# Kernel optimization log

Hardware: AMD Instinct MI355X
Metric: run time of the kernel (lower is better)

The kernel has to match this reference:

```python
import jax, jax.numpy as jnp
import numpy as np
import math

WS = 8           # window size
NUM_HEADS = 8
LN_EPS = 1e-5


def window_partition(x, ws):
    # x: [B, H, W, C] -> [B*nH*nW, ws, ws, C]
    B, H, W, C = x.shape
    x = x.reshape(B, H // ws, ws, W // ws, ws, C)
    return x.transpose(0, 1, 3, 2, 4, 5).reshape(-1, ws, ws, C)


def window_reverse(w, ws, H, W):
    # w: [B*nH*nW, ws, ws, C] -> [B, H, W, C]
    B = w.shape[0] // ((H // ws) * (W // ws))
    x = w.reshape(B, H // ws, W // ws, ws, ws, -1)
    return x.transpose(0, 1, 3, 2, 4, 5).reshape(B, H, W, -1)


def layernorm(x, g, b):
    mu = jnp.mean(x, axis=-1, keepdims=True)
    var = jnp.mean(jnp.square(x - mu), axis=-1, keepdims=True)
    return (x - mu) * jax.lax.rsqrt(var + LN_EPS) * g + b


def rotation_grid(H, W, ws):
    """Vectorized rotation_process lookup table -> sampling grid [H, W, 2]=(lat,lon)."""
    nH, nW = H // ws, W // ws
    r = 1.0 / ws
    seq = -1.0 + r + 2.0 * r * jnp.arange(ws, dtype=jnp.float32)  # make_coord centers
    ch, cw = jnp.meshgrid(seq, seq, indexing='ij')
    t0 = ch.reshape(-1) / nH                       # [ws*ws] latitude template
    t1 = cw.reshape(-1) / nW                       # [ws*ws] longitude template
    beta = (2.0 * (jnp.arange(nH, dtype=jnp.float32) + 0.5) / nH - 1.0) * (math.pi / 2)  # [nH]
    th = t0 * (math.pi / 2) + math.pi / 2
    ph = t1 * math.pi
    sb, cb = jnp.sin(beta)[:, None], jnp.cos(beta)[:, None]
    st, ct = jnp.sin(th)[None, :], jnp.cos(th)[None, :]
    sp, cp = jnp.sin(ph)[None, :], jnp.cos(ph)[None, :]
    new_th = jnp.arccos(-sb * st * cp + cb * ct)                    # [nH, ws*ws]
    new_ph = jnp.arctan2(st * sp, cb * st * cp + sb * ct)
    lat = jnp.clip((new_th - math.pi / 2) / (math.pi / 2), -1.0, 1.0)
    lon = new_ph / math.pi
    shift = 2.0 * (0.5 - (jnp.arange(nW, dtype=jnp.float32) + 0.5) / nW)
    lon = lon[:, None, :] - shift[None, :, None]                    # [nH, nW, ws*ws]
    lon = jnp.where(lon > 1.0, lon - 2.0, lon)
    lon = jnp.where(lon < -1.0, lon + 2.0, lon)
    lat = jnp.broadcast_to(lat[:, None, :], lon.shape)
    g = jnp.stack([lat, lon], axis=-1).reshape(nH, nW, ws, ws, 2)
    return g.transpose(0, 2, 1, 3, 4).reshape(H, W, 2)


def grid_sample_nearest(im, grid):
    """F.grid_sample(mode='nearest', align_corners=False, padding='zeros').
    im: [B, H, W, C]; grid: [H, W, 2]=(y,x) normalized; shared across batch."""
    B, H, W, C = im.shape
    gy, gx = grid[..., 0], grid[..., 1]
    iy = jnp.round(((gy + 1.0) * H - 1.0) / 2.0).astype(jnp.int32)
    ix = jnp.round(((gx + 1.0) * W - 1.0) / 2.0).astype(jnp.int32)
    valid = (iy >= 0) & (iy < H) & (ix >= 0) & (ix < W)
    iyc = jnp.clip(iy, 0, H - 1)
    ixc = jnp.clip(ix, 0, W - 1)
    out = im[:, iyc, ixc, :]                                        # [B, H, W, C]
    return out * valid[None, :, :, None].astype(im.dtype)


def dwconv3x3(x, w, b):
    # x: [B, C, H, W], w: [C, 1, 3, 3] depthwise
    y = jax.lax.conv_general_dilated(x, w, (1, 1), 'SAME',
                                     feature_group_count=x.shape[1],
                                     dimension_numbers=('NCHW', 'OIHW', 'NCHW'))
    return y + b[None, :, None, None]


def setup_inputs() -> dict:
    key = jax.random.key(0)
    B, H, W, C, dff = 8, 64, 128, 256, 1024
    ks = jax.random.split(key, 10)
    s = 0.02
    return {
        'x': jax.random.normal(ks[0], (B, H * W, C), jnp.float32),
        'H': H, 'W': W,
        'norm1_g': jnp.ones((C,), jnp.float32),
        'norm1_b': jnp.zeros((C,), jnp.float32),
        'wq': jax.random.normal(ks[1], (C, C), jnp.float32) * s,
        'bq': jnp.zeros((C,), jnp.float32),
        'wk': jax.random.normal(ks[2], (C, C), jnp.float32) * s,
        'bk': jnp.zeros((C,), jnp.float32),
        'wv': jax.random.normal(ks[3], (C, C), jnp.float32) * s,
        'bv': jnp.zeros((C,), jnp.float32),
        'rpe_w': jax.random.normal(ks[4], (C, 1, 3, 3), jnp.float32) * s,
        'rpe_b': jnp.zeros((C,), jnp.float32),
        'proj_w': jax.random.normal(ks[5], (C, C), jnp.float32) * s,
        'proj_b': jnp.zeros((C,), jnp.float32),
        'norm2_g': jnp.ones((C,), jnp.float32),
        'norm2_b': jnp.zeros((C,), jnp.float32),
        'fc1_w': jax.random.normal(ks[6], (C, dff), jnp.float32) * s,
        'fc1_b': jnp.zeros((dff,), jnp.float32),
        'fc2_w': jax.random.normal(ks[7], (dff, C), jnp.float32) * s,
        'fc2_b': jnp.zeros((C,), jnp.float32),
    }


def reference(x, H, W, norm1_g, norm1_b, wq, bq, wk, bk, wv, bv, rpe_w, rpe_b,
              proj_w, proj_b, norm2_g, norm2_b, fc1_w, fc1_b, fc2_w, fc2_b):
    B, L, C = x.shape
    ws, nh = WS, NUM_HEADS
    hd = C // nh
    scale = hd ** (-0.5)
    N = ws * ws

    shortcut = x
    xn = layernorm(x, norm1_g, norm1_b).reshape(B, H, W, C)
    # panoramic rotation of the key features (rotation_process)
    y = grid_sample_nearest(xn, rotation_grid(H, W, ws))

    xw = window_partition(xn, ws).reshape(-1, N, C)   # [Bw, N, C]
    yw = window_partition(y, ws).reshape(-1, N, C)
    Bw = xw.shape[0]

    q = xw @ wq + bq
    # depthwise-conv positional term on window-reversed q (rpe_table)
    qimg = window_reverse(q.reshape(-1, ws, ws, C), ws, H, W).transpose(0, 3, 1, 2)  # [B,C,H,W]
    lepe = window_partition(dwconv3x3(qimg, rpe_w, rpe_b).transpose(0, 2, 3, 1), ws).reshape(-1, N, C)

    k = yw @ wk + bk
    v = xw @ wv + bv
    qh = q.reshape(Bw, N, nh, hd).transpose(0, 2, 1, 3) * scale   # [Bw,h,N,d]
    kh = k.reshape(Bw, N, nh, hd).transpose(0, 2, 1, 3)
    vh = v.reshape(Bw, N, nh, hd).transpose(0, 2, 1, 3)
    attn = jax.nn.softmax(jnp.einsum('bhnd,bhmd->bhnm', qh, kh), axis=-1)
    out = jnp.einsum('bhnm,bhmd->bhnd', attn, vh).transpose(0, 2, 1, 3).reshape(Bw, N, C)
    out = (out + lepe) @ proj_w + proj_b

    x = shortcut + window_reverse(out.reshape(-1, ws, ws, C), ws, H, W).reshape(B, L, C)
    h = layernorm(x, norm2_g, norm2_b)
    h = jax.nn.gelu(h @ fc1_w + fc1_b, approximate=False) @ fc2_w + fc2_b
    return x + h
```

## Files before the change

### kernel.cpp

```cpp
#include <hip/hip_runtime.h>

typedef __bf16 bf16;
typedef __bf16 bf16x4 __attribute__((ext_vector_type(4)));
typedef __bf16 bf16x8 __attribute__((ext_vector_type(8)));
typedef float  f32x4  __attribute__((ext_vector_type(4)));

#define HH   64
#define WW   128
#define CC   256
#define MTOK 65536
#define PI_D 3.14159265358979323846

__device__ __forceinline__ int win_row(int b, int h, int w) {
  return ((b * 8 + (h >> 3)) * 16 + (w >> 3)) * 64 + ((h & 7) << 3) + (w & 7);
}

__device__ __forceinline__ void gl_lds16(const bf16* g, bf16* l) {
  __builtin_amdgcn_global_load_lds(
      (const __attribute__((address_space(1))) unsigned int*)g,
      (__attribute__((address_space(3))) unsigned int*)l, 16, 0, 0);
}

__global__ __launch_bounds__(256) void grid_kernel(int* __restrict__ wmap,
                                                   bf16* __restrict__ zrow,
                                                   float* __restrict__ biasqv,
                                                   const float* __restrict__ bq,
                                                   const float* __restrict__ bv) {
  int p = blockIdx.x * 256 + threadIdx.x;
  if (p < 256) zrow[p] = (bf16)0.0f;
  if (p < 512) biasqv[p] = (p < 256) ? bq[p] : bv[p - 256];
  if (p >= HH * WW) return;
  int h = p >> 7, w = p & 127;
  int bh = h >> 3, i = h & 7, bw = w >> 3, j = w & 7;
  double seq_i = -0.875 + 0.25 * i;
  double seq_j = -0.875 + 0.25 * j;
  double t0 = seq_i / 8.0, t1 = seq_j / 16.0;
  double beta = ((bh + 0.5) / 4.0 - 1.0) * (PI_D / 2.0);
  double th = t0 * (PI_D / 2.0) + PI_D / 2.0;
  double ph = t1 * PI_D;
  double sb = sin(beta), cb = cos(beta);
  double st = sin(th),  ct = cos(th);
  double sp = sin(ph),  cp = cos(ph);
  double arg = -sb * st * cp + cb * ct;
  arg = fmin(1.0, fmax(-1.0, arg));
  double nth = acos(arg);
  double nph = atan2(st * sp, cb * st * cp + sb * ct);
  double lat = (nth - PI_D / 2.0) / (PI_D / 2.0);
  lat = fmin(1.0, fmax(-1.0, lat));
  double shift = 1.0 - (2.0 * bw + 1.0) / 16.0;
  double lon = nph / PI_D - shift;
  if (lon > 1.0) lon -= 2.0; else if (lon < -1.0) lon += 2.0;
  int iy = (int)rint(((lat + 1.0) * (double)HH - 1.0) * 0.5);
  int ix = (int)rint(((lon + 1.0) * (double)WW - 1.0) * 0.5);
  bool valid = (iy >= 0 && iy < HH && ix >= 0 && ix < WW);
  int dwr = ((h >> 3) * 16 + (w >> 3)) * 64 + ((h & 7) << 3) + (w & 7);
  int src = valid ? (((iy >> 3) * 16 + (ix >> 3)) * 64 + ((iy & 7) << 3) + (ix & 7)) : -1;
  wmap[dwr] = src;
}

__global__ __launch_bounds__(256) void convert_wt(const float* __restrict__ src,
                                                  bf16* __restrict__ dst,
                                                  int K, int N) {
  __shared__ float tile[32][33];
  int bk = blockIdx.x * 32, bn = blockIdx.y * 32;
  int tx = threadIdx.x & 31, ty = threadIdx.x >> 5;
#pragma unroll
  for (int r = 0; r < 4; r++)
    tile[ty + 8 * r][tx] = src[(size_t)(bk + ty + 8 * r) * N + bn + tx];
  __syncthreads();
#pragma unroll
  for (int r = 0; r < 4; r++)
    dst[(size_t)(bn + ty + 8 * r) * K + bk + tx] = (bf16)tile[tx][ty + 8 * r];
}

__global__ __launch_bounds__(256) void ln_kernel(const float* __restrict__ x,
                                                 const float* __restrict__ g,
                                                 const float* __restrict__ bta,
                                                 bf16* __restrict__ out,
                                                 int permute) {
  int token = blockIdx.x * 4 + (threadIdx.x >> 6);
  int lane = threadIdx.x & 63;
  const float4 v = *(const float4*)(x + (size_t)token * CC + lane * 4);
  float s  = v.x + v.y + v.z + v.w;
  float ss = v.x * v.x + v.y * v.y + v.z * v.z + v.w * v.w;
#pragma unroll
  for (int o = 32; o > 0; o >>= 1) {
    s  += __shfl_xor(s, o);
    ss += __shfl_xor(ss, o);
  }
  float mu = s * (1.0f / CC);
  float var = ss * (1.0f / CC) - mu * mu;
  float rs = rsqrtf(var + 1e-5f);
  int row = token;
  if (permute) {
    int b = token >> 13, l = token & 8191;
    row = win_row(b, l >> 7, l & 127);
  }
  int c = lane * 4;
  const float4 gv = *(const float4*)(g + c);
  const float4 bv = *(const float4*)(bta + c);
  bf16x4 o4;
  o4[0] = (bf16)((v.x - mu) * rs * gv.x + bv.x);
  o4[1] = (bf16)((v.y - mu) * rs * gv.y + bv.y);
  o4[2] = (bf16)((v.z - mu) * rs * gv.z + bv.z);
  o4[3] = (bf16)((v.w - mu) * rs * gv.w + bv.w);
  *(bf16x4*)(out + (size_t)row * CC + c) = o4;
}

#define EPI_BF16 0
#define EPI_GELU 1
#define EPI_PROJ 2
#define EPI_FC2  3

template <int EPI, bool GATHER>
__global__ __launch_bounds__(256) void gemm_bt(const bf16* __restrict__ A,
                                               const bf16* __restrict__ Bt,
                                               const float* __restrict__ bias,
                                               bf16* __restrict__ outB,
                                               float* __restrict__ outF,
                                               const float* __restrict__ res,
                                               const int* __restrict__ amap,
                                               const bf16* __restrict__ zrow,
                                               int M, int N, int K) {
  __shared__ bf16 lA[128 * 32];
  __shared__ bf16 lB[128 * 32];
  const int t = threadIdx.x;
  const int wave = t >> 6, lane = t & 63;
  const int quad = lane >> 4, l16 = lane & 15;
  const int mb = blockIdx.y, nb = blockIdx.x;
  const int wm = wave >> 1, wn = wave & 1;

  f32x4 acc[4][4];
#pragma unroll
  for (int i = 0; i < 4; i++)
#pragma unroll
    for (int j = 0; j < 4; j++)
#pragma unroll
      for (int r = 0; r < 4; r++) acc[i][j][r] = 0.0f;

  const int arow = t >> 2;
  const int acol = (t & 3) << 3;
  const bf16 *gA, *gA2;
  if (GATHER) {
    int r1 = mb * 128 + arow;
    int b1 = r1 >> 13, s1 = amap[r1 & 8191];
    gA = (s1 >= 0) ? A + ((size_t)((b1 << 13) + s1)) * K + acol : zrow + acol;
    int r2 = r1 + 64;
    int b2 = r2 >> 13, s2 = amap[r2 & 8191];
    gA2 = (s2 >= 0) ? A + ((size_t)((b2 << 13) + s2)) * K + acol : zrow + acol;
  } else {
    gA = A + (size_t)(mb * 128 + arow) * K + acol;
    gA2 = gA + (size_t)64 * K;
  }
  const bf16* gB  = Bt + (size_t)(nb * 128 + arow) * K + acol;
  const bf16* gB2 = gB + (size_t)64 * K;
  bf16* lAp  = &lA[t * 8];
  bf16* lBp  = &lB[t * 8];
  bf16* lAp2 = &lA[2048 + t * 8];
  bf16* lBp2 = &lB[2048 + t * 8];

  for (int kk = 0; kk < K; kk += 32) {
    __syncthreads();
    gl_lds16(gA + kk, lAp);
    gl_lds16(gA2 + kk, lAp2);
    gl_lds16(gB + kk, lBp);
    gl_lds16(gB2 + kk, lBp2);
    __syncthreads();
    bf16x8 af[4], bfr[4];
#pragma unroll
    for (int i = 0; i < 4; i++)
      af[i] = *(const bf16x8*)&lA[(wm * 64 + i * 16 + l16) * 32 + quad * 8];
#pragma unroll
    for (int j = 0; j < 4; j++)
      bfr[j] = *(const bf16x8*)&lB[(wn * 64 + j * 16 + l16) * 32 + quad * 8];
#pragma unroll
    for (int i = 0; i < 4; i++)
#pragma unroll
      for (int j = 0; j < 4; j++)
        acc[i][j] = __builtin_amdgcn_mfma_f32_16x16x32_bf16(af[i], bfr[j], acc[i][j], 0, 0, 0);
  }

  const int m0 = mb * 128 + wm * 64;
  const int n0 = nb * 128 + wn * 64;
#pragma unroll
  for (int i = 0; i < 4; i++) {
#pragma unroll
    for (int j = 0; j < 4; j++) {
      const int col = n0 + j * 16 + l16;
      const int rowb = m0 + i * 16 + quad * 4;
      const float bsv = bias[col];
#pragma unroll
      for (int r = 0; r < 4; r++) {
        const int row = rowb + r;
        float v = acc[i][j][r] + bsv;
        if (EPI == EPI_BF16) {
          outB[(size_t)row * N + col] = (bf16)v;
        } else if (EPI == EPI_GELU) {
          float gl = 0.5f * v * (1.0f + erff(v * 0.70710678118654752f));
          outB[(size_t)row * N + col] = (bf16)gl;
        } else if (EPI == EPI_FC2) {
          size_t idx = (size_t)row * N + col;
          outF[idx] = res[idx] + v;
        } else {
          int wi = row >> 6, tt = row & 63;
          int b = wi >> 7, hb = (wi >> 4) & 7, wb = wi & 15;
          int h = hb * 8 + (tt >> 3), w = wb * 8 + (tt & 7);
          size_t idx = ((size_t)(b * 8192 + h * 128 + w)) * 256 + col;
          outF[idx] = res[idx] + v;
        }
      }
    }
  }
}

__global__ __launch_bounds__(256) void lepe_kernel(const bf16* __restrict__ qv,
                                                   const float* __restrict__ rw,
                                                   const float* __restrict__ rb,
                                                   bf16* __restrict__ ao) {
  __shared__ __align__(16) bf16 hq[100 * 256];
  const int blk = blockIdx.x;
  const int b = blk >> 7, hb = (blk >> 4) & 7, wb = blk & 15;
  const int t = threadIdx.x;
  const int h0 = hb * 8 - 1, w0 = wb * 8 - 1;

  for (int idx = t; idx < 3200; idx += 256) {
    int pix = idx >> 5, ch = (idx & 31) * 8;
    int pi = pix / 10, pj = pix - pi * 10;
    int h = h0 + pi, w = w0 + pj;
    bf16x8 val;
#pragma unroll
    for (int e = 0; e < 8; e++) val[e] = (bf16)0.0f;
    if (h >= 0 && h < HH && w >= 0 && w < WW)
      val = *(const bf16x8*)(qv + (size_t)win_row(b, h, w) * 512 + ch);
    *(bf16x8*)(&hq[pix * 256 + ch]) = val;
  }
  __syncthreads();

  const int cg = t & 31, c0 = cg * 8;
  const int i = t >> 5;

  float wr[9][8];
#pragma unroll
  for (int e = 0; e < 8; e++)
#pragma unroll
    for (int tap = 0; tap < 9; tap++) wr[tap][e] = rw[(c0 + e) * 9 + tap];
  float bias[8];
  *(float4*)&bias[0] = *(const float4*)(rb + c0);
  *(float4*)&bias[4] = *(const float4*)(rb + c0 + 4);

  float cur[3][3][8];
#pragma unroll
  for (int rr = 0; rr < 3; rr++)
#pragma unroll
    for (int cc = 0; cc < 2; cc++) {
      bf16x8 v = *(const bf16x8*)(&hq[((i + rr) * 10 + cc) * 256 + c0]);
#pragma unroll
      for (int e = 0; e < 8; e++) cur[rr][cc][e] = (float)v[e];
    }

#pragma unroll
  for (int j = 0; j < 8; j++) {
    const int snew = (j + 2) % 3;
#pragma unroll
    for (int rr = 0; rr < 3; rr++) {
      bf16x8 v = *(const bf16x8*)(&hq[((i + rr) * 10 + (j + 2)) * 256 + c0]);
#pragma unroll
      for (int e = 0; e < 8; e++) cur[rr][snew][e] = (float)v[e];
    }
    float acc[8];
#pragma unroll
    for (int e = 0; e < 8; e++) acc[e] = bias[e];
#pragma unroll
    for (int rr = 0; rr < 3; rr++)
#pragma unroll
      for (int dc = 0; dc < 3; dc++) {
        const int slot = (j + dc) % 3;
        const int tap = rr * 3 + dc;
#pragma unroll
        for (int e = 0; e < 8; e++) acc[e] += cur[rr][slot][e] * wr[tap][e];
      }
    bf16x8 o;
#pragma unroll
    for (int e = 0; e < 8; e++) o[e] = (bf16)acc[e];
    *(bf16x8*)(ao + (size_t)(blk * 64 + i * 8 + j) * 256 + c0) = o;
  }
}

#define SP 72

__global__ __launch_bounds__(256) void attn_kernel(const bf16* __restrict__ qv,
                                                   const bf16* __restrict__ kb,
                                                   bf16* __restrict__ ao) {
  __shared__ __align__(16) bf16 Pl[4][64 * SP];
  const int wave = threadIdx.x >> 6, lane = threadIdx.x & 63;
  const int quad = lane >> 4, l16 = lane & 15;
  const size_t rowbase = (size_t)(blockIdx.x >> 1) * 64;
  const int head = ((blockIdx.x & 1) << 2) + wave;
  const int hc = head * 32;
  bf16* P = Pl[wave];
  const float scale = 0.17677669529663687f;

  bf16x8 aq[4], bk4[4];
#pragma unroll
  for (int mi = 0; mi < 4; mi++)
    aq[mi] = *(const bf16x8*)(qv + (rowbase + mi * 16 + l16) * 512 + hc + quad * 8);
#pragma unroll
  for (int ni = 0; ni < 4; ni++)
    bk4[ni] = *(const bf16x8*)(kb + (rowbase + ni * 16 + l16) * 256 + hc + quad * 8);
  f32x4 sacc[4][4];
#pragma unroll
  for (int mi = 0; mi < 4; mi++)
#pragma unroll
    for (int ni = 0; ni < 4; ni++)
#pragma unroll
      for (int r = 0; r < 4; r++) sacc[mi][ni][r] = 0.0f;
#pragma unroll
  for (int mi = 0; mi < 4; mi++)
#pragma unroll
    for (int ni = 0; ni < 4; ni++)
      sacc[mi][ni] = __builtin_amdgcn_mfma_f32_16x16x32_bf16(aq[mi], bk4[ni], sacc[mi][ni], 0, 0, 0);

  bf16x8 vb2[2][2];
#pragma unroll
  for (int n0 = 0; n0 < 2; n0++)
#pragma unroll
    for (int kc = 0; kc < 2; kc++) {
      const bf16* vp = qv + (rowbase + kc * 32 + quad * 8) * 512 + 256 + hc + n0 * 16 + l16;
#pragma unroll
      for (int j = 0; j < 8; j++) vb2[n0][kc][j] = vp[(size_t)j * 512];
    }

#pragma unroll
  for (int mi = 0; mi < 4; mi++) {
#pragma unroll
    for (int r = 0; r < 4; r++) {
      float mx = -1e30f;
#pragma unroll
      for (int ni = 0; ni < 4; ni++) mx = fmaxf(mx, sacc[mi][ni][r]);
      mx = fmaxf(mx, __shfl_xor(mx, 1));
      mx = fmaxf(mx, __shfl_xor(mx, 2));
      mx = fmaxf(mx, __shfl_xor(mx, 4));
      mx = fmaxf(mx, __shfl_xor(mx, 8));
      float sm = 0.0f;
#pragma unroll
      for (int ni = 0; ni < 4; ni++) {
        float e = expf(scale * (sacc[mi][ni][r] - mx));
        sacc[mi][ni][r] = e;
        sm += e;
      }
      sm += __shfl_xor(sm, 1);
      sm += __shfl_xor(sm, 2);
      sm += __shfl_xor(sm, 4);
      sm += __shfl_xor(sm, 8);
      float inv = 1.0f / sm;
#pragma unroll
      for (int ni = 0; ni < 4; ni++) sacc[mi][ni][r] *= inv;
    }
#pragma unroll
    for (int ni = 0; ni < 4; ni++)
#pragma unroll
      for (int r = 0; r < 4; r++)
        P[(mi * 16 + quad * 4 + r) * SP + ni * 16 + l16] = (bf16)sacc[mi][ni][r];
  }

  f32x4 oacc[4][2];
#pragma unroll
  for (int mi = 0; mi < 4; mi++)
#pragma unroll
    for (int n0 = 0; n0 < 2; n0++)
#pragma unroll
      for (int r = 0; r < 4; r++) oacc[mi][n0][r] = 0.0f;
#pragma unroll
  for (int mi = 0; mi < 4; mi++)
#pragma unroll
    for (int kc = 0; kc < 2; kc++) {
      bf16x8 pf = *(const bf16x8*)&P[(mi * 16 + l16) * SP + kc * 32 + quad * 8];
#pragma unroll
      for (int n0 = 0; n0 < 2; n0++)
        oacc[mi][n0] = __builtin_amdgcn_mfma_f32_16x16x32_bf16(pf, vb2[n0][kc], oacc[mi][n0], 0, 0, 0);
    }

#pragma unroll
  for (int mi = 0; mi < 4; mi++)
#pragma unroll
    for (int n0 = 0; n0 < 2; n0++)
#pragma unroll
      for (int r = 0; r < 4; r++) {
        size_t idx = (rowbase + mi * 16 + quad * 4 + r) * CC + hc + n0 * 16 + l16;
        ao[idx] = (bf16)((float)ao[idx] + oacc[mi][n0][r]);
      }
}

extern "C" void kernel_launch(void* const* d_in, const int* in_sizes, int n_in,
                              void* d_out, int out_size, void* d_ws, size_t ws_size,
                              hipStream_t stream) {
  const float* x     = (const float*)d_in[0];
  const float* n1g   = (const float*)d_in[3];
  const float* n1b   = (const float*)d_in[4];
  const float* wq    = (const float*)d_in[5];
  const float* bq    = (const float*)d_in[6];
  const float* wk    = (const float*)d_in[7];
  const float* bk    = (const float*)d_in[8];
  const float* wv    = (const float*)d_in[9];
  const float* bv    = (const float*)d_in[10];
  const float* rpe_w = (const float*)d_in[11];
  const float* rpe_b = (const float*)d_in[12];
  const float* pw    = (const float*)d_in[13];
  const float* pb    = (const float*)d_in[14];
  const float* n2g   = (const float*)d_in[15];
  const float* n2b   = (const float*)d_in[16];
  const float* f1w   = (const float*)d_in[17];
  const float* f1b   = (const float*)d_in[18];
  const float* f2w   = (const float*)d_in[19];
  const float* f2b   = (const float*)d_in[20];
  float* out = (float*)d_out;
  char* ws = (char*)d_ws;

  const size_t A_ = 33554432ull;
  bf16* xw  = (bf16*)(ws);
  bf16* ao  = (bf16*)(ws);
  bf16* xh  = (bf16*)(ws);
  bf16* qv  = (bf16*)(ws + A_);
  bf16* h1  = (bf16*)(ws + A_);
  bf16* kb  = (bf16*)d_out;
  char* wsp = ws + 3 * A_;
  bf16* wqvT = (bf16*)(wsp);
  bf16* wkT  = (bf16*)(wsp + 262144);
  bf16* pwT  = (bf16*)(wsp + 393216);
  bf16* f1T  = (bf16*)(wsp + 524288);
  bf16* f2T  = (bf16*)(wsp + 1048576);
  float* biasqv = (float*)(wsp + 1572864);
  int*   wmap   = (int*)(wsp + 1574912);
  bf16*  zrow   = (bf16*)(wsp + 1607680);

  convert_wt<<<dim3(8, 8),  256, 0, stream>>>(wq,  wqvT,          256, 256);
  convert_wt<<<dim3(8, 8),  256, 0, stream>>>(wv,  wqvT + 65536,  256, 256);
  convert_wt<<<dim3(8, 8),  256, 0, stream>>>(wk,  wkT,           256, 256);
  convert_wt<<<dim3(8, 8),  256, 0, stream>>>(pw,  pwT,           256, 256);
  convert_wt<<<dim3(8, 32), 256, 0, stream>>>(f1w, f1T,           256, 1024);
  convert_wt<<<dim3(32, 8), 256, 0, stream>>>(f2w, f2T,           1024, 256);
  grid_kernel<<<32, 256, 0, stream>>>(wmap, zrow, biasqv, bq, bv);

  ln_kernel<<<MTOK / 4, 256, 0, stream>>>(x, n1g, n1b, xw, 1);

  gemm_bt<EPI_BF16, false><<<dim3(4, 512), 256, 0, stream>>>(
      xw, wqvT, biasqv, qv, nullptr, nullptr, nullptr, nullptr, MTOK, 512, 256);
  gemm_bt<EPI_BF16, true><<<dim3(2, 512), 256, 0, stream>>>(
      xw, wkT, bk, kb, nullptr, nullptr, wmap, zrow, MTOK, 256, 256);

  lepe_kernel<<<1024, 256, 0, stream>>>(qv, rpe_w, rpe_b, ao);
  attn_kernel<<<2048, 256, 0, stream>>>(qv, kb, ao);

  gemm_bt<EPI_PROJ, false><<<dim3(2, 512), 256, 0, stream>>>(
      ao, pwT, pb, nullptr, out, x, nullptr, nullptr, MTOK, 256, 256);

  ln_kernel<<<MTOK / 4, 256, 0, stream>>>(out, n2g, n2b, xh, 0);

  const int CH = 32768;
  for (int c = 0; c < 2; c++) {
    gemm_bt<EPI_GELU, false><<<dim3(8, CH / 128), 256, 0, stream>>>(
        xh + (size_t)c * CH * 256, f1T, f1b, h1, nullptr, nullptr, nullptr, nullptr,
        CH, 1024, 256);
    gemm_bt<EPI_FC2, false><<<dim3(2, CH / 128), 256, 0, stream>>>(
        h1, f2T, f2b, nullptr, out + (size_t)c * CH * 256, out + (size_t)c * CH * 256,
        nullptr, nullptr, CH, 256, 1024);
  }
}
```

Before: 517.7 us.

## Store V transposed per window and stage attention output through LDS

```diff
diff --git a/kernel.cpp b/kernel.cpp
--- a/kernel.cpp
+++ b/kernel.cpp
@@ -111,6 +111,7 @@
 #define EPI_GELU 1
 #define EPI_PROJ 2
 #define EPI_FC2  3
+#define EPI_QV   4
 
 template <int EPI, bool GATHER>
 __global__ __launch_bounds__(256) void gemm_bt(const bf16* __restrict__ A,
@@ -121,6 +122,7 @@
                                                const float* __restrict__ res,
                                                const int* __restrict__ amap,
                                                const bf16* __restrict__ zrow,
+                                               bf16* __restrict__ outB2,
                                                int M, int N, int K) {
   __shared__ bf16 lA[128 * 32];
   __shared__ bf16 lB[128 * 32];
@@ -195,6 +197,12 @@
         float v = acc[i][j][r] + bsv;
         if (EPI == EPI_BF16) {
           outB[(size_t)row * N + col] = (bf16)v;
+        } else if (EPI == EPI_QV) {
+          if (col < 256) {
+            outB[(size_t)row * 256 + col] = (bf16)v;
+          } else {
+            outB2[((size_t)(row >> 6) * 256 + (col - 256)) * 64 + (row & 63)] = (bf16)v;
+          }
         } else if (EPI == EPI_GELU) {
           float gl = 0.5f * v * (1.0f + erff(v * 0.70710678118654752f));
           outB[(size_t)row * N + col] = (bf16)gl;
@@ -213,7 +221,7 @@
   }
 }
 
-__global__ __launch_bounds__(256) void lepe_kernel(const bf16* __restrict__ qv,
+__global__ __launch_bounds__(256) void lepe_kernel(const bf16* __restrict__ qb,
                                                    const float* __restrict__ rw,
                                                    const float* __restrict__ rb,
                                                    bf16* __restrict__ ao) {
@@ -231,7 +239,7 @@
 #pragma unroll
     for (int e = 0; e < 8; e++) val[e] = (bf16)0.0f;
     if (h >= 0 && h < HH && w >= 0 && w < WW)
-      val = *(const bf16x8*)(qv + (size_t)win_row(b, h, w) * 512 + ch);
+      val = *(const bf16x8*)(qb + (size_t)win_row(b, h, w) * 256 + ch);
     *(bf16x8*)(&hq[pix * 256 + ch]) = val;
   }
   __syncthreads();
@@ -286,15 +294,17 @@
   }
 }
 
-#define SP 72
-
-__global__ __launch_bounds__(256) void attn_kernel(const bf16* __restrict__ qv,
+#define SP 74
+
+__global__ __launch_bounds__(256) void attn_kernel(const bf16* __restrict__ qb,
                                                    const bf16* __restrict__ kb,
+                                                   const bf16* __restrict__ vt,
                                                    bf16* __restrict__ ao) {
   __shared__ __align__(16) bf16 Pl[4][64 * SP];
   const int wave = threadIdx.x >> 6, lane = threadIdx.x & 63;
   const int quad = lane >> 4, l16 = lane & 15;
-  const size_t rowbase = (size_t)(blockIdx.x >> 1) * 64;
+  const int win = blockIdx.x >> 1;
+  const size_t rowbase = (size_t)win * 64;
   const int head = ((blockIdx.x & 1) << 2) + wave;
   const int hc = head * 32;
   bf16* P = Pl[wave];
@@ -303,7 +313,7 @@
   bf16x8 aq[4], bk4[4];
 #pragma unroll
   for (int mi = 0; mi < 4; mi++)
-    aq[mi] = *(const bf16x8*)(qv + (rowbase + mi * 16 + l16) * 512 + hc + quad * 8);
+    aq[mi] = *(const bf16x8*)(qb + (rowbase + mi * 16 + l16) * 256 + hc + quad * 8);
 #pragma unroll
   for (int ni = 0; ni < 4; ni++)
     bk4[ni] = *(const bf16x8*)(kb + (rowbase + ni * 16 + l16) * 256 + hc + quad * 8);
@@ -324,11 +334,9 @@
 #pragma unroll
   for (int n0 = 0; n0 < 2; n0++)
 #pragma unroll
-    for (int kc = 0; kc < 2; kc++) {
-      const bf16* vp = qv + (rowbase + kc * 32 + quad * 8) * 512 + 256 + hc + n0 * 16 + l16;
-#pragma unroll
-      for (int j = 0; j < 8; j++) vb2[n0][kc][j] = vp[(size_t)j * 512];
-    }
+    for (int kc = 0; kc < 2; kc++)
+      vb2[n0][kc] = *(const bf16x8*)(vt + ((size_t)win * 256 + hc + n0 * 16 + l16) * 64 +
+                                     kc * 32 + quad * 8);
 
 #pragma unroll
   for (int mi = 0; mi < 4; mi++) {
@@ -380,15 +388,25 @@
         oacc[mi][n0] = __builtin_amdgcn_mfma_f32_16x16x32_bf16(pf, vb2[n0][kc], oacc[mi][n0], 0, 0, 0);
     }
 
+  bf16* Ol = P;
 #pragma unroll
   for (int mi = 0; mi < 4; mi++)
 #pragma unroll
     for (int n0 = 0; n0 < 2; n0++)
 #pragma unroll
-      for (int r = 0; r < 4; r++) {
-        size_t idx = (rowbase + mi * 16 + quad * 4 + r) * CC + hc + n0 * 16 + l16;
-        ao[idx] = (bf16)((float)ao[idx] + oacc[mi][n0][r]);
-      }
+      for (int r = 0; r < 4; r++)
+        Ol[(mi * 16 + quad * 4 + r) * 34 + n0 * 16 + l16] = (bf16)oacc[mi][n0][r];
+
+  bf16* aop = ao + (rowbase + lane) * 256 + hc;
+#pragma unroll
+  for (int cc = 0; cc < 4; cc++) {
+    bf16x8 ov = *(const bf16x8*)&Ol[lane * 34 + cc * 8];
+    bf16x8 lp = *(const bf16x8*)(aop + cc * 8);
+    bf16x8 so;
+#pragma unroll
+    for (int e = 0; e < 8; e++) so[e] = (bf16)((float)ov[e] + (float)lp[e]);
+    *(bf16x8*)(aop + cc * 8) = so;
+  }
 }
 
 extern "C" void kernel_launch(void* const* d_in, const int* in_sizes, int n_in,
@@ -420,7 +438,8 @@
   bf16* xw  = (bf16*)(ws);
   bf16* ao  = (bf16*)(ws);
   bf16* xh  = (bf16*)(ws);
-  bf16* qv  = (bf16*)(ws + A_);
+  bf16* qb  = (bf16*)(ws + A_);
+  bf16* vt  = (bf16*)(ws + 2 * A_);
   bf16* h1  = (bf16*)(ws + A_);
   bf16* kb  = (bf16*)d_out;
   char* wsp = ws + 3 * A_;
@@ -443,26 +462,26 @@
 
   ln_kernel<<<MTOK / 4, 256, 0, stream>>>(x, n1g, n1b, xw, 1);
 
-  gemm_bt<EPI_BF16, false><<<dim3(4, 512), 256, 0, stream>>>(
-      xw, wqvT, biasqv, qv, nullptr, nullptr, nullptr, nullptr, MTOK, 512, 256);
+  gemm_bt<EPI_QV, false><<<dim3(4, 512), 256, 0, stream>>>(
+      xw, wqvT, biasqv, qb, nullptr, nullptr, nullptr, nullptr, vt, MTOK, 512, 256);
   gemm_bt<EPI_BF16, true><<<dim3(2, 512), 256, 0, stream>>>(
-      xw, wkT, bk, kb, nullptr, nullptr, wmap, zrow, MTOK, 256, 256);
-
-  lepe_kernel<<<1024, 256, 0, stream>>>(qv, rpe_w, rpe_b, ao);
-  attn_kernel<<<2048, 256, 0, stream>>>(qv, kb, ao);
+      xw, wkT, bk, kb, nullptr, nullptr, wmap, zrow, nullptr, MTOK, 256, 256);
+
+  lepe_kernel<<<1024, 256, 0, stream>>>(qb, rpe_w, rpe_b, ao);
+  attn_kernel<<<2048, 256, 0, stream>>>(qb, kb, vt, ao);
 
   gemm_bt<EPI_PROJ, false><<<dim3(2, 512), 256, 0, stream>>>(
-      ao, pwT, pb, nullptr, out, x, nullptr, nullptr, MTOK, 256, 256);
+      ao, pwT, pb, nullptr, out, x, nullptr, nullptr, nullptr, MTOK, 256, 256);
 
   ln_kernel<<<MTOK / 4, 256, 0, stream>>>(out, n2g, n2b, xh, 0);
 
   const int CH = 32768;
   for (int c = 0; c < 2; c++) {
     gemm_bt<EPI_GELU, false><<<dim3(8, CH / 128), 256, 0, stream>>>(
-        xh + (size_t)c * CH * 256, f1T, f1b, h1, nullptr, nullptr, nullptr, nullptr,
+        xh + (size_t)c * CH * 256, f1T, f1b, h1, nullptr, nullptr, nullptr, nullptr, nullptr,
         CH, 1024, 256);
     gemm_bt<EPI_FC2, false><<<dim3(2, CH / 128), 256, 0, stream>>>(
         h1, f2T, f2b, nullptr, out + (size_t)c * CH * 256, out + (size_t)c * CH * 256,
-        nullptr, nullptr, CH, 256, 1024);
-  }
-}
+        nullptr, nullptr, nullptr, CH, 256, 1024);
+  }
+}
```

After: 549.4 us. +6.1%, slower.
